# Optimization experiments

Measured on AMD Instinct MI355X. Metric: run time of the kernel, lower is better.

Reference implementation:

```python
import jax, jax.numpy as jnp
import numpy as np

B, T, H, A = 64, 512, 1024, 300


def setup_inputs() -> dict:
    key = jax.random.key(0)
    ks = jax.random.split(key, 12)
    s = 0.02  # weight init scale
    return {
        "hidden": jax.random.normal(ks[0], (B, T, H), jnp.float32),
        "aspect": jax.random.normal(ks[1], (B, 1, A), jnp.float32),
        # torch Linear stores weight as [out_features, in_features]
        "W_h": jax.random.normal(ks[2], (H, H), jnp.float32) * s,
        "b_h": jax.random.normal(ks[3], (H,), jnp.float32) * s,
        "W_v": jax.random.normal(ks[4], (A, A), jnp.float32) * s,
        "b_v": jax.random.normal(ks[5], (A,), jnp.float32) * s,
        "w_w": jax.random.normal(ks[6], (1, H + A), jnp.float32) * s,
        "w_b": jax.random.normal(ks[7], (1,), jnp.float32) * s,
        "W_p": jax.random.normal(ks[8], (H, H), jnp.float32) * s,
        "b_p": jax.random.normal(ks[9], (H,), jnp.float32) * s,
        "W_x": jax.random.normal(ks[10], (H, H), jnp.float32) * s,
        "b_x": jax.random.normal(ks[11], (H,), jnp.float32) * s,
    }


def reference(hidden, aspect, W_h, b_h, W_v, b_v, w_w, w_b, W_p, b_p, W_x, b_x):
    # transformed aspect: [B, 1, A], repeated along seq dim -> [B, T, A]
    tv = aspect @ W_v.T + b_v
    rep_v = jnp.broadcast_to(tv, (hidden.shape[0], hidden.shape[1], tv.shape[-1]))
    # M = tanh(concat(W_h(hidden), repeated_v)) : [B, T, H+A]
    M = jnp.tanh(jnp.concatenate([hidden @ W_h.T + b_h, rep_v], axis=-1))
    # additive attention scores -> softmax over T
    scores = jnp.einsum("bts,os->bto", M, w_w)[..., 0] + w_b[0]  # [B, T]
    alpha = jax.nn.softmax(scores, axis=-1)
    # weighted sum r = alpha^T @ hidden : [B, 1, H]
    r = jnp.einsum("bt,bth->bh", alpha, hidden)[:, None, :]
    # NOTE: faithful to original torch broadcasting quirk:
    # [B,1,H] + [B,H] broadcasts to [B,B,H]
    output = jnp.tanh((r @ W_p.T + b_p) + (hidden[:, -1, :] @ W_x.T + b_x))
    return output
```

## Files before the change

kernel.cpp:

```cpp
#include <hip/hip_runtime.h>
#include <hip/hip_bf16.h>
#include <stdint.h>

#define B_DIM 64
#define T_DIM 512
#define H_DIM 1024
#define K_DIM 1024
#define M_DIM (B_DIM * T_DIM)

typedef __bf16 bf16x8 __attribute__((ext_vector_type(8)));
typedef float f32x4 __attribute__((ext_vector_type(4)));

__device__ __forceinline__ float tanh_fast(float x) {
  float e = __expf(2.0f * x);
  return 1.0f - 2.0f / (e + 1.0f);
}

__device__ __forceinline__ float bf2f(unsigned short u) {
  return __uint_as_float(((unsigned int)u) << 16);
}

__device__ __forceinline__ void async_cp16(const void* gp, void* lp) {
  __builtin_amdgcn_global_load_lds(
      reinterpret_cast<const __attribute__((address_space(1))) uint32_t*>(
          reinterpret_cast<uintptr_t>(gp)),
      reinterpret_cast<__attribute__((address_space(3))) uint32_t*>(
          reinterpret_cast<uintptr_t>(lp)),
      16, 0, 0);
}

__global__ void cvt_hidden_kernel(const float* __restrict__ src, __bf16* __restrict__ dst) {
  int i = blockIdx.x * 256 + threadIdx.x;
  float4 v = reinterpret_cast<const float4*>(src)[i];
  union { __bf16 b[4]; uint2 u; } o;
  o.b[0] = (__bf16)v.x; o.b[1] = (__bf16)v.y; o.b[2] = (__bf16)v.z; o.b[3] = (__bf16)v.w;
  reinterpret_cast<uint2*>(dst)[i] = o.u;
}

__global__ void cvtW_zero_kernel(const float* __restrict__ Wh, __bf16* __restrict__ whBf,
                                 float* __restrict__ scores, float* __restrict__ r) {
  int bid = blockIdx.x, tid = threadIdx.x;
  if (bid < 1024) {
    int i = bid * 256 + tid;
    float4 v = reinterpret_cast<const float4*>(Wh)[i];
    union { __bf16 b[4]; uint2 u; } o;
    o.b[0] = (__bf16)v.x; o.b[1] = (__bf16)v.y; o.b[2] = (__bf16)v.z; o.b[3] = (__bf16)v.w;
    reinterpret_cast<uint2*>(whBf)[i] = o.u;
  } else if (bid < 1056) {
    int i = (bid - 1024) * 256 + tid;
    reinterpret_cast<float4*>(scores)[i] = make_float4(0.f, 0.f, 0.f, 0.f);
  } else {
    int i = (bid - 1056) * 256 + tid;
    reinterpret_cast<float4*>(r)[i] = make_float4(0.f, 0.f, 0.f, 0.f);
  }
}

#define GM_BK 64
__global__ __launch_bounds__(256, 2) void gemm_scores_kernel(
    const __bf16* __restrict__ A, const __bf16* __restrict__ Bm,
    const float* __restrict__ bh, const float* __restrict__ ww,
    float* __restrict__ scores) {
  __shared__ __attribute__((aligned(16))) __bf16 lA[256 * GM_BK];
  __shared__ __attribute__((aligned(16))) __bf16 lB[128 * GM_BK];

  const int tid = threadIdx.x;
  const int bid = blockIdx.x;
  const int m0 = (bid & 127) * 256;
  const int n0 = (bid >> 7) * 128;

  const int wv = tid >> 6;
  const int lane = tid & 63;
  const int wm = wv & 1, wn = wv >> 1;
  const int r16 = lane & 15, quad = lane >> 4;

  f32x4 acc[8][4] = {};

  const __bf16* gA[8]; __bf16* lAd[8];
#pragma unroll
  for (int j = 0; j < 8; ++j) {
    int c = j * 256 + tid;
    int row = c >> 3;
    int p = c & 7;
    int kc = p ^ ((row >> 1) & 7);
    gA[j] = A + (size_t)(m0 + row) * K_DIM + kc * 8;
    lAd[j] = &lA[c * 8];
  }
  const __bf16* gB[4]; __bf16* lBd[4];
#pragma unroll
  for (int j = 0; j < 4; ++j) {
    int c = j * 256 + tid;
    int row = c >> 3;
    int p = c & 7;
    int kc = p ^ ((row >> 1) & 7);
    gB[j] = Bm + (size_t)(n0 + row) * K_DIM + kc * 8;
    lBd[j] = &lB[c * 8];
  }

  const int sw = r16 >> 1;
  const __bf16* pa[2]; const __bf16* pb[2];
#pragma unroll
  for (int kk = 0; kk < 2; ++kk) {
    pa[kk] = &lA[(wm * 128 + r16) * GM_BK + ((kk * 4 + quad) ^ sw) * 8];
    pb[kk] = &lB[(wn * 64 + r16) * GM_BK + ((kk * 4 + quad) ^ sw) * 8];
  }

#pragma unroll
  for (int k0 = 0; k0 < K_DIM; k0 += GM_BK) {
#pragma unroll
    for (int j = 0; j < 8; ++j) async_cp16(gA[j] + k0, lAd[j]);
#pragma unroll
    for (int j = 0; j < 4; ++j) async_cp16(gB[j] + k0, lBd[j]);
    __syncthreads();
#pragma unroll
    for (int kk = 0; kk < 2; ++kk) {
      bf16x8 bfr[4];
#pragma unroll
      for (int ni = 0; ni < 4; ++ni)
        bfr[ni] = *reinterpret_cast<const bf16x8*>(pb[kk] + ni * 16 * GM_BK);
      bf16x8 af[8];
#pragma unroll
      for (int mi = 0; mi < 8; ++mi)
        af[mi] = *reinterpret_cast<const bf16x8*>(pa[kk] + mi * 16 * GM_BK);
#pragma unroll
      for (int mi = 0; mi < 8; ++mi)
#pragma unroll
        for (int ni = 0; ni < 4; ++ni)
          acc[mi][ni] = __builtin_amdgcn_mfma_f32_16x16x32_bf16(af[mi], bfr[ni], acc[mi][ni], 0, 0, 0);
    }
    __syncthreads();
  }

  float bhv[4], wwv[4];
#pragma unroll
  for (int ni = 0; ni < 4; ++ni) {
    int n = n0 + wn * 64 + ni * 16 + r16;
    bhv[ni] = bh[n];
    wwv[ni] = ww[n];
  }
#pragma unroll
  for (int mi = 0; mi < 8; ++mi) {
#pragma unroll
    for (int rg = 0; rg < 4; ++rg) {
      float s = 0.f;
#pragma unroll
      for (int ni = 0; ni < 4; ++ni)
        s += tanh_fast(acc[mi][ni][rg] + bhv[ni]) * wwv[ni];
      s += __shfl_xor(s, 1, 16);
      s += __shfl_xor(s, 2, 16);
      s += __shfl_xor(s, 4, 16);
      s += __shfl_xor(s, 8, 16);
      if (r16 == 0) {
        int m = m0 + wm * 128 + mi * 16 + quad * 4 + rg;
        atomicAdd(&scores[m], s);
      }
    }
  }
}

__global__ void wsum_kernel(const float* __restrict__ scores,
                            const __bf16* __restrict__ hiddenBf,
                            float* __restrict__ r) {
  __shared__ float al[64];
  __shared__ float red[8];
  const int bid = blockIdx.x, tid = threadIdx.x;
  const int b = bid >> 3, tc = bid & 7;
  const int wv = tid >> 6, lane = tid & 63;
  float v0 = scores[b * T_DIM + tid];
  float v1 = scores[b * T_DIM + 256 + tid];
  float mx = fmaxf(v0, v1);
#pragma unroll
  for (int off = 1; off < 64; off <<= 1) mx = fmaxf(mx, __shfl_xor(mx, off, 64));
  if (lane == 0) red[wv] = mx;
  __syncthreads();
  mx = fmaxf(fmaxf(red[0], red[1]), fmaxf(red[2], red[3]));
  float e0 = __expf(v0 - mx), e1 = __expf(v1 - mx);
  float s = e0 + e1;
#pragma unroll
  for (int off = 1; off < 64; off <<= 1) s += __shfl_xor(s, off, 64);
  if (lane == 0) red[4 + wv] = s;
  __syncthreads();
  float inv = 1.0f / (red[4] + red[5] + red[6] + red[7]);
  if (tid < 64) al[tid] = __expf(scores[b * T_DIM + tc * 64 + tid] - mx) * inv;
  __syncthreads();
  const __bf16* hp = hiddenBf + (size_t)b * T_DIM * H_DIM + (size_t)tc * 64 * H_DIM + tid * 4;
  float4 acc = make_float4(0.f, 0.f, 0.f, 0.f);
#pragma unroll 8
  for (int t = 0; t < 64; ++t) {
    float a = al[t];
    ushort4 u = *reinterpret_cast<const ushort4*>(hp + (size_t)t * H_DIM);
    acc.x += a * bf2f(u.x);
    acc.y += a * bf2f(u.y);
    acc.z += a * bf2f(u.z);
    acc.w += a * bf2f(u.w);
  }
  float* rp = r + b * H_DIM + tid * 4;
  atomicAdd(rp + 0, acc.x);
  atomicAdd(rp + 1, acc.y);
  atomicAdd(rp + 2, acc.z);
  atomicAdd(rp + 3, acc.w);
}

__global__ void rowvec_matT_kernel(const float* __restrict__ src, size_t src_stride,
                                   const float* __restrict__ W, const float* __restrict__ bias,
                                   float* __restrict__ dst) {
  __shared__ float sv[H_DIM];
  const int i = blockIdx.y, h0 = blockIdx.x * 64, tid = threadIdx.x;
  reinterpret_cast<float4*>(sv)[tid] =
      reinterpret_cast<const float4*>(src + (size_t)i * src_stride)[tid];
  __syncthreads();
  const int hl = tid >> 2;
  const int kq = tid & 3;
  const float* wr = W + (size_t)(h0 + hl) * H_DIM + kq * 256;
  const float* svp = sv + kq * 256;
  float acc = 0.f;
#pragma unroll 4
  for (int k = 0; k < 256; k += 4) {
    float4 w4 = *reinterpret_cast<const float4*>(wr + k);
    float4 s4 = *reinterpret_cast<const float4*>(svp + k);
    acc += w4.x * s4.x + w4.y * s4.y + w4.z * s4.z + w4.w * s4.w;
  }
  acc += __shfl_xor(acc, 1, 4);
  acc += __shfl_xor(acc, 2, 4);
  if (kq == 0) dst[(size_t)i * H_DIM + h0 + hl] = acc + bias[h0 + hl];
}

__global__ void final_kernel(const float* __restrict__ rp, const float* __restrict__ xq,
                             float* __restrict__ out) {
  int idx = blockIdx.x * 256 + threadIdx.x;
  int e = idx * 4;
  int i = e >> 16;
  int j = (e >> 10) & 63;
  int h = e & 1023;
  float4 a = *reinterpret_cast<const float4*>(&rp[i * H_DIM + h]);
  float4 b = *reinterpret_cast<const float4*>(&xq[j * H_DIM + h]);
  float4 o;
  o.x = tanh_fast(a.x + b.x);
  o.y = tanh_fast(a.y + b.y);
  o.z = tanh_fast(a.z + b.z);
  o.w = tanh_fast(a.w + b.w);
  *reinterpret_cast<float4*>(&out[e]) = o;
}

extern "C" void kernel_launch(void* const* d_in, const int* in_sizes, int n_in,
                              void* d_out, int out_size, void* d_ws, size_t ws_size,
                              hipStream_t stream) {
  const float* hidden = (const float*)d_in[0];
  const float* W_h = (const float*)d_in[2];
  const float* b_h = (const float*)d_in[3];
  const float* w_w = (const float*)d_in[6];
  const float* W_p = (const float*)d_in[8];
  const float* b_p = (const float*)d_in[9];
  const float* W_x = (const float*)d_in[10];
  const float* b_x = (const float*)d_in[11];
  float* out = (float*)d_out;

  char* ws = (char*)d_ws;
  __bf16* hidBf = (__bf16*)ws;
  __bf16* whBf = (__bf16*)(ws + 67108864);
  float* scores = (float*)(ws + 69206016);
  float* r = (float*)(ws + 69468160);
  float* rp = (float*)(ws + 69730304);
  float* xq = (float*)(ws + 69992448);

  cvt_hidden_kernel<<<M_DIM * H_DIM / 1024, 256, 0, stream>>>(hidden, hidBf);
  cvtW_zero_kernel<<<1120, 256, 0, stream>>>(W_h, whBf, scores, r);

  gemm_scores_kernel<<<1024, 256, 0, stream>>>(hidBf, whBf, b_h, w_w, scores);

  wsum_kernel<<<512, 256, 0, stream>>>(scores, hidBf, r);

  rowvec_matT_kernel<<<dim3(H_DIM / 64, B_DIM), 256, 0, stream>>>(r, (size_t)H_DIM, W_p, b_p, rp);
  rowvec_matT_kernel<<<dim3(H_DIM / 64, B_DIM), 256, 0, stream>>>(
      hidden + (size_t)(T_DIM - 1) * H_DIM, (size_t)T_DIM * H_DIM, W_x, b_x, xq);

  final_kernel<<<(B_DIM * B_DIM * H_DIM / 4) / 256, 256, 0, stream>>>(rp, xq, out);
}
```

Baseline: 379.8 us.

## Merge prep kernels, replace atomics with partials, batch rowvec GEMVs into one launch

Merges the hidden and W_h bf16 conversions and the zeroing into a single prep launch. wsum now writes per-chunk partial sums into an r8 buffer, reusing whBf's space after the GEMM, instead of atomically adding into r. The two rowvec GEMV launches become one kernel with a z-dimension for W_p and W_x. Each block handles 4 rows so every weight load is reused four times, and the r partials are reduced during staging. This cuts launch count, atomics, and weight re-reads, but it relies on whBf being dead before wsum writes over it.

```diff
diff --git a/kernel.cpp b/kernel.cpp
--- a/kernel.cpp
+++ b/kernel.cpp
@@ -29,29 +29,25 @@
       16, 0, 0);
 }
 
-__global__ void cvt_hidden_kernel(const float* __restrict__ src, __bf16* __restrict__ dst) {
-  int i = blockIdx.x * 256 + threadIdx.x;
-  float4 v = reinterpret_cast<const float4*>(src)[i];
-  union { __bf16 b[4]; uint2 u; } o;
-  o.b[0] = (__bf16)v.x; o.b[1] = (__bf16)v.y; o.b[2] = (__bf16)v.z; o.b[3] = (__bf16)v.w;
-  reinterpret_cast<uint2*>(dst)[i] = o.u;
-}
-
-__global__ void cvtW_zero_kernel(const float* __restrict__ Wh, __bf16* __restrict__ whBf,
-                                 float* __restrict__ scores, float* __restrict__ r) {
-  int bid = blockIdx.x, tid = threadIdx.x;
-  if (bid < 1024) {
+__global__ void prep_kernel(const float* __restrict__ hidden, __bf16* __restrict__ hidBf,
+                            const float* __restrict__ Wh, __bf16* __restrict__ whBf,
+                            float* __restrict__ scores) {
+  const int bid = blockIdx.x, tid = threadIdx.x;
+  if (bid < 32768) {
     int i = bid * 256 + tid;
+    float4 v = reinterpret_cast<const float4*>(hidden)[i];
+    union { __bf16 b[4]; uint2 u; } o;
+    o.b[0] = (__bf16)v.x; o.b[1] = (__bf16)v.y; o.b[2] = (__bf16)v.z; o.b[3] = (__bf16)v.w;
+    reinterpret_cast<uint2*>(hidBf)[i] = o.u;
+  } else if (bid < 33792) {
+    int i = (bid - 32768) * 256 + tid;
     float4 v = reinterpret_cast<const float4*>(Wh)[i];
     union { __bf16 b[4]; uint2 u; } o;
     o.b[0] = (__bf16)v.x; o.b[1] = (__bf16)v.y; o.b[2] = (__bf16)v.z; o.b[3] = (__bf16)v.w;
     reinterpret_cast<uint2*>(whBf)[i] = o.u;
-  } else if (bid < 1056) {
-    int i = (bid - 1024) * 256 + tid;
+  } else {
+    int i = (bid - 33792) * 256 + tid;
     reinterpret_cast<float4*>(scores)[i] = make_float4(0.f, 0.f, 0.f, 0.f);
-  } else {
-    int i = (bid - 1056) * 256 + tid;
-    reinterpret_cast<float4*>(r)[i] = make_float4(0.f, 0.f, 0.f, 0.f);
   }
 }
 
@@ -159,7 +155,7 @@
 
 __global__ void wsum_kernel(const float* __restrict__ scores,
                             const __bf16* __restrict__ hiddenBf,
-                            float* __restrict__ r) {
+                            float* __restrict__ r8) {
   __shared__ float al[64];
   __shared__ float red[8];
   const int bid = blockIdx.x, tid = threadIdx.x;
@@ -193,35 +189,68 @@
     acc.z += a * bf2f(u.z);
     acc.w += a * bf2f(u.w);
   }
-  float* rp = r + b * H_DIM + tid * 4;
-  atomicAdd(rp + 0, acc.x);
-  atomicAdd(rp + 1, acc.y);
-  atomicAdd(rp + 2, acc.z);
-  atomicAdd(rp + 3, acc.w);
-}
-
-__global__ void rowvec_matT_kernel(const float* __restrict__ src, size_t src_stride,
-                                   const float* __restrict__ W, const float* __restrict__ bias,
-                                   float* __restrict__ dst) {
-  __shared__ float sv[H_DIM];
-  const int i = blockIdx.y, h0 = blockIdx.x * 64, tid = threadIdx.x;
-  reinterpret_cast<float4*>(sv)[tid] =
-      reinterpret_cast<const float4*>(src + (size_t)i * src_stride)[tid];
+  *reinterpret_cast<float4*>(r8 + (size_t)(b * 8 + tc) * H_DIM + tid * 4) = acc;
+}
+
+#define IG 4
+__global__ void rowvec2_kernel(const float* __restrict__ r8,
+                               const float* __restrict__ hidden,
+                               const float* __restrict__ W_p, const float* __restrict__ b_p,
+                               const float* __restrict__ W_x, const float* __restrict__ b_x,
+                               float* __restrict__ rp, float* __restrict__ xq) {
+  __shared__ __attribute__((aligned(16))) float sv[IG][H_DIM];
+  const int h0 = blockIdx.x * 64;
+  const int i0 = blockIdx.y * IG;
+  const int which = blockIdx.z;
+  const int tid = threadIdx.x;
+  const float* W = which ? W_x : W_p;
+  const float* bias = which ? b_x : b_p;
+  float* dst = which ? xq : rp;
+  if (which == 0) {
+#pragma unroll
+    for (int ii = 0; ii < IG; ++ii) {
+      const float* src = r8 + (size_t)(i0 + ii) * 8 * H_DIM + tid * 4;
+      float4 a = *reinterpret_cast<const float4*>(src);
+#pragma unroll
+      for (int tc = 1; tc < 8; ++tc) {
+        float4 v = *reinterpret_cast<const float4*>(src + (size_t)tc * H_DIM);
+        a.x += v.x; a.y += v.y; a.z += v.z; a.w += v.w;
+      }
+      *reinterpret_cast<float4*>(&sv[ii][tid * 4]) = a;
+    }
+  } else {
+#pragma unroll
+    for (int ii = 0; ii < IG; ++ii) {
+      const float* src = hidden + (size_t)(i0 + ii) * T_DIM * H_DIM +
+                         (size_t)(T_DIM - 1) * H_DIM + tid * 4;
+      *reinterpret_cast<float4*>(&sv[ii][tid * 4]) = *reinterpret_cast<const float4*>(src);
+    }
+  }
   __syncthreads();
   const int hl = tid >> 2;
   const int kq = tid & 3;
-  const float* wr = W + (size_t)(h0 + hl) * H_DIM + kq * 256;
-  const float* svp = sv + kq * 256;
-  float acc = 0.f;
-#pragma unroll 4
-  for (int k = 0; k < 256; k += 4) {
-    float4 w4 = *reinterpret_cast<const float4*>(wr + k);
-    float4 s4 = *reinterpret_cast<const float4*>(svp + k);
-    acc += w4.x * s4.x + w4.y * s4.y + w4.z * s4.z + w4.w * s4.w;
-  }
-  acc += __shfl_xor(acc, 1, 4);
-  acc += __shfl_xor(acc, 2, 4);
-  if (kq == 0) dst[(size_t)i * H_DIM + h0 + hl] = acc + bias[h0 + hl];
+  const float* wr = W + (size_t)(h0 + hl) * H_DIM + kq * 4;
+  float acc[IG] = {};
+#pragma unroll 8
+  for (int j = 0; j < 64; ++j) {
+    float4 w4 = *reinterpret_cast<const float4*>(wr + j * 16);
+#pragma unroll
+    for (int ii = 0; ii < IG; ++ii) {
+      float4 s4 = *reinterpret_cast<const float4*>(&sv[ii][kq * 4 + j * 16]);
+      acc[ii] += w4.x * s4.x + w4.y * s4.y + w4.z * s4.z + w4.w * s4.w;
+    }
+  }
+#pragma unroll
+  for (int ii = 0; ii < IG; ++ii) {
+    acc[ii] += __shfl_xor(acc[ii], 1, 4);
+    acc[ii] += __shfl_xor(acc[ii], 2, 4);
+  }
+  if (kq == 0) {
+    float bb = bias[h0 + hl];
+#pragma unroll
+    for (int ii = 0; ii < IG; ++ii)
+      dst[(size_t)(i0 + ii) * H_DIM + h0 + hl] = acc[ii] + bb;
+  }
 }
 
 __global__ void final_kernel(const float* __restrict__ rp, const float* __restrict__ xq,
@@ -257,21 +286,19 @@
   char* ws = (char*)d_ws;
   __bf16* hidBf = (__bf16*)ws;
   __bf16* whBf = (__bf16*)(ws + 67108864);
+  float* r8 = (float*)(ws + 67108864);
   float* scores = (float*)(ws + 69206016);
-  float* r = (float*)(ws + 69468160);
-  float* rp = (float*)(ws + 69730304);
-  float* xq = (float*)(ws + 69992448);
-
-  cvt_hidden_kernel<<<M_DIM * H_DIM / 1024, 256, 0, stream>>>(hidden, hidBf);
-  cvtW_zero_kernel<<<1120, 256, 0, stream>>>(W_h, whBf, scores, r);
+  float* rpB = (float*)(ws + 69337088);
+  float* xqB = (float*)(ws + 69599232);
+
+  prep_kernel<<<33824, 256, 0, stream>>>(hidden, hidBf, W_h, whBf, scores);
 
   gemm_scores_kernel<<<1024, 256, 0, stream>>>(hidBf, whBf, b_h, w_w, scores);
 
-  wsum_kernel<<<512, 256, 0, stream>>>(scores, hidBf, r);
-
-  rowvec_matT_kernel<<<dim3(H_DIM / 64, B_DIM), 256, 0, stream>>>(r, (size_t)H_DIM, W_p, b_p, rp);
-  rowvec_matT_kernel<<<dim3(H_DIM / 64, B_DIM), 256, 0, stream>>>(
-      hidden + (size_t)(T_DIM - 1) * H_DIM, (size_t)T_DIM * H_DIM, W_x, b_x, xq);
-
-  final_kernel<<<(B_DIM * B_DIM * H_DIM / 4) / 256, 256, 0, stream>>>(rp, xq, out);
-}
+  wsum_kernel<<<512, 256, 0, stream>>>(scores, hidBf, r8);
+
+  rowvec2_kernel<<<dim3(H_DIM / 64, B_DIM / IG, 2), 256, 0, stream>>>(
+      r8, hidden, W_p, b_p, W_x, b_x, rpB, xqB);
+
+  final_kernel<<<(B_DIM * B_DIM * H_DIM / 4) / 256, 256, 0, stream>>>(rpB, xqB, out);
+}
```

New measurement: 344.3 us. 1.1x faster.
